# Performance work log

Measured on AMD Instinct MI355X. Metric: run time of the kernel, lower is better.

The kernel has to match this reference:

```python
import jax, jax.numpy as jnp
import numpy as np

SHIFT_HZ = 20.0
SAMPLE_RATE = 16000
N_FFT = 512
SHIFT_BINS = SHIFT_HZ / (SAMPLE_RATE / N_FFT)  # 0.64 bins
EPS = 1e-08


def setup_inputs() -> dict:
    key = jax.random.key(0)
    # log-magnitude spectrogram [B, 1, F, T]
    x = jax.random.normal(key, (32, 1, 257, 4096), dtype=jnp.float32)
    return {"x": x}


def reference(x):
    B, C, F, T = x.shape
    x_lin = jnp.power(10.0, x[:, 0])  # [B, F, T] linear magnitude

    f = jnp.arange(F, dtype=jnp.float32)
    target = f + SHIFT_BINS                     # source bin (fractional)
    f_low = jnp.floor(target)
    f_high = jnp.ceil(target)
    alpha = (target - f_low).astype(x.dtype)    # interp weight; 0 when integer

    valid = (target >= 0) & (target < F) & (f_low < F) & (f_high < F)
    lo = jnp.clip(f_low.astype(jnp.int32), 0, F - 1)
    hi = jnp.clip(f_high.astype(jnp.int32), 0, F - 1)

    # gather along frequency axis + linear interp (alpha==0 reduces to copy)
    interp = ((1.0 - alpha)[None, :, None] * jnp.take(x_lin, lo, axis=1)
              + alpha[None, :, None] * jnp.take(x_lin, hi, axis=1))
    shifted = jnp.where(valid[None, :, None], interp, 0.0)

    return jnp.log10(shifted + EPS)[:, None]    # [B, 1, F, T]
```

## Files before the change

kernel.cpp:

```cpp
#include <hip/hip_runtime.h>

#define B_DIM 32
#define F_DIM 257
#define T_DIM 4096
#define EPS_F 1e-8f

#define LOG2_10  3.32192809488736234787f
#define LOG10_2  0.30102999566398119521f

typedef float f32x4 __attribute__((ext_vector_type(4)));

__device__ __forceinline__ float pow10_fast(float v) {
    return __builtin_amdgcn_exp2f(v * LOG2_10);
}

__device__ __forceinline__ float log10_fast(float v) {
    return __builtin_amdgcn_logf(v) * LOG10_2;
}

__global__ __launch_bounds__(256) void freq_shift_kernel(
        const float* __restrict__ x, float* __restrict__ out) {
    const int bf = blockIdx.x;
    const int f  = bf % F_DIM;
    const long long base = (long long)bf * T_DIM;
    const int tid = threadIdx.x;

    f32x4* __restrict__ orow = (f32x4*)(out + base);

    if (f == F_DIM - 1) {
        const float cv = log10_fast(EPS_F);
        f32x4 v;
        v.x = cv; v.y = cv; v.z = cv; v.w = cv;
#pragma unroll
        for (int i = 0; i < T_DIM / 4 / 256; ++i)
            __builtin_nontemporal_store(v, orow + i * 256 + tid);
        return;
    }

    const f32x4* __restrict__ row0 = (const f32x4*)(x + base);
    const f32x4* __restrict__ row1 = (const f32x4*)(x + base + T_DIM);

    const float ff     = (float)f;
    const float target = ff + 0.64f;
    const float alpha  = target - ff;
    const float beta   = 1.0f - alpha;

    f32x4 va[4], vb[4];
#pragma unroll
    for (int i = 0; i < 4; ++i) va[i] = row0[i * 256 + tid];
#pragma unroll
    for (int i = 0; i < 4; ++i) vb[i] = row1[i * 256 + tid];

#pragma unroll
    for (int i = 0; i < 4; ++i) {
        f32x4 r;
        r.x = log10_fast(beta * pow10_fast(va[i].x) + alpha * pow10_fast(vb[i].x) + EPS_F);
        r.y = log10_fast(beta * pow10_fast(va[i].y) + alpha * pow10_fast(vb[i].y) + EPS_F);
        r.z = log10_fast(beta * pow10_fast(va[i].z) + alpha * pow10_fast(vb[i].z) + EPS_F);
        r.w = log10_fast(beta * pow10_fast(va[i].w) + alpha * pow10_fast(vb[i].w) + EPS_F);
        __builtin_nontemporal_store(r, orow + i * 256 + tid);
    }
}

extern "C" void kernel_launch(void* const* d_in, const int* in_sizes, int n_in,
                              void* d_out, int out_size, void* d_ws, size_t ws_size,
                              hipStream_t stream) {
    const float* x = (const float*)d_in[0];
    float* out = (float*)d_out;
    dim3 grid(B_DIM * F_DIM);
    dim3 block(256);
    freq_shift_kernel<<<grid, block, 0, stream>>>(x, out);
}
```

Before: 224.3 us.

## Tile 8 frequency rows per block to reuse pow10 and loads, remap blocks across XCDs

Each block now processes 8 consecutive frequency rows over half the time axis. It loads 9 input rows once and carries the pow10 of the previous row forward, so every input row is read and exponentiated once instead of twice. Block IDs are remapped so that contiguous work chunks land on the same XCD, which aims to improve L2 locality. The cost is more registers per thread and far fewer blocks (2048 instead of 8224), which may reduce latency hiding.

```diff
diff --git a/kernel.cpp b/kernel.cpp
--- a/kernel.cpp
+++ b/kernel.cpp
@@ -8,57 +8,78 @@
 #define LOG2_10  3.32192809488736234787f
 #define LOG10_2  0.30102999566398119521f
 
+#define ROWS 8
+#define FBLKS 32
+#define TCHUNKS 2
+#define TCHUNK_F (T_DIM / TCHUNKS)
+#define ROWV (T_DIM / 4)
+#define NBLK (B_DIM * FBLKS * TCHUNKS)
+#define XCD_CHUNK (NBLK / 8)
+
 typedef float f32x4 __attribute__((ext_vector_type(4)));
 
 __device__ __forceinline__ float pow10_fast(float v) {
     return __builtin_amdgcn_exp2f(v * LOG2_10);
 }
-
 __device__ __forceinline__ float log10_fast(float v) {
     return __builtin_amdgcn_logf(v) * LOG10_2;
+}
+__device__ __forceinline__ f32x4 pow10_4(f32x4 v) {
+    f32x4 r;
+    r.x = pow10_fast(v.x); r.y = pow10_fast(v.y);
+    r.z = pow10_fast(v.z); r.w = pow10_fast(v.w);
+    return r;
 }
 
 __global__ __launch_bounds__(256) void freq_shift_kernel(
         const float* __restrict__ x, float* __restrict__ out) {
-    const int bf = blockIdx.x;
-    const int f  = bf % F_DIM;
-    const long long base = (long long)bf * T_DIM;
+    const int bid = blockIdx.x;
+    const int id  = (bid & 7) * XCD_CHUNK + (bid >> 3);
+
+    const int b   = id >> 6;
+    const int rem = id & 63;
+    const int tc  = rem >> 5;
+    const int fb  = rem & 31;
+    const int f0  = fb * ROWS;
     const int tid = threadIdx.x;
 
-    f32x4* __restrict__ orow = (f32x4*)(out + base);
+    const long long base = ((long long)(b * F_DIM + f0)) * T_DIM + (long long)tc * TCHUNK_F;
+    const f32x4* __restrict__ xin = (const f32x4*)(x + base);
+    f32x4*       __restrict__ o   = (f32x4*)(out + base);
 
-    if (f == F_DIM - 1) {
-        const float cv = log10_fast(EPS_F);
-        f32x4 v;
-        v.x = cv; v.y = cv; v.z = cv; v.w = cv;
 #pragma unroll
-        for (int i = 0; i < T_DIM / 4 / 256; ++i)
-            __builtin_nontemporal_store(v, orow + i * 256 + tid);
-        return;
+    for (int half = 0; half < 2; ++half) {
+        const int c = tid + half * 256;
+
+        f32x4 v[ROWS + 1];
+#pragma unroll
+        for (int r = 0; r <= ROWS; ++r) v[r] = xin[r * ROWV + c];
+
+        f32x4 pprev = pow10_4(v[0]);
+#pragma unroll
+        for (int r = 0; r < ROWS; ++r) {
+            const float ff    = (float)(f0 + r);
+            const float alpha = (ff + 0.64f) - ff;
+            const float beta  = 1.0f - alpha;
+
+            const f32x4 pcur = pow10_4(v[r + 1]);
+            f32x4 res;
+            res.x = log10_fast(beta * pprev.x + alpha * pcur.x + EPS_F);
+            res.y = log10_fast(beta * pprev.y + alpha * pcur.y + EPS_F);
+            res.z = log10_fast(beta * pprev.z + alpha * pcur.z + EPS_F);
+            res.w = log10_fast(beta * pprev.w + alpha * pcur.w + EPS_F);
+            __builtin_nontemporal_store(res, o + r * ROWV + c);
+            pprev = pcur;
+        }
     }
 
-    const f32x4* __restrict__ row0 = (const f32x4*)(x + base);
-    const f32x4* __restrict__ row1 = (const f32x4*)(x + base + T_DIM);
-
-    const float ff     = (float)f;
-    const float target = ff + 0.64f;
-    const float alpha  = target - ff;
-    const float beta   = 1.0f - alpha;
-
-    f32x4 va[4], vb[4];
-#pragma unroll
-    for (int i = 0; i < 4; ++i) va[i] = row0[i * 256 + tid];
-#pragma unroll
-    for (int i = 0; i < 4; ++i) vb[i] = row1[i * 256 + tid];
-
-#pragma unroll
-    for (int i = 0; i < 4; ++i) {
-        f32x4 r;
-        r.x = log10_fast(beta * pow10_fast(va[i].x) + alpha * pow10_fast(vb[i].x) + EPS_F);
-        r.y = log10_fast(beta * pow10_fast(va[i].y) + alpha * pow10_fast(vb[i].y) + EPS_F);
-        r.z = log10_fast(beta * pow10_fast(va[i].z) + alpha * pow10_fast(vb[i].z) + EPS_F);
-        r.w = log10_fast(beta * pow10_fast(va[i].w) + alpha * pow10_fast(vb[i].w) + EPS_F);
-        __builtin_nontemporal_store(r, orow + i * 256 + tid);
+    if (fb == FBLKS - 1) {
+        const float cv = log10_fast(EPS_F);
+        f32x4 vv; vv.x = cv; vv.y = cv; vv.z = cv; vv.w = cv;
+        f32x4* orow = (f32x4*)(out + ((long long)(b * F_DIM + 256)) * T_DIM
+                               + (long long)tc * TCHUNK_F);
+        __builtin_nontemporal_store(vv, orow + tid);
+        __builtin_nontemporal_store(vv, orow + tid + 256);
     }
 }
 
@@ -67,7 +88,7 @@
                               hipStream_t stream) {
     const float* x = (const float*)d_in[0];
     float* out = (float*)d_out;
-    dim3 grid(B_DIM * F_DIM);
+    dim3 grid(NBLK);
     dim3 block(256);
     freq_shift_kernel<<<grid, block, 0, stream>>>(x, out);
 }
```

Measured after the change: 237.0 us. 5.7% more time.

## Process four rows per block with double-buffered loads and XCD-aware block mapping

Applied to the files above, without the earlier changes.

Each block now handles four consecutive frequency rows and issues the loads for the next row before computing the current one, hiding memory latency. Block IDs are remapped so each XCD gets a contiguous chunk of rows. Adjacent rows, which share an input row, then hit the same L2. The cost is fewer blocks in flight and more registers per thread for the double buffers, which may lower occupancy.

```diff
diff --git a/kernel.cpp b/kernel.cpp
--- a/kernel.cpp
+++ b/kernel.cpp
@@ -8,57 +8,76 @@
 #define LOG2_10  3.32192809488736234787f
 #define LOG10_2  0.30102999566398119521f
 
+#define TASKS 4
+#define NBLK  (B_DIM * F_DIM / TASKS)
+#define ROWV  (T_DIM / 4)
+#define XCD_CHUNK (NBLK / 8)
+
 typedef float f32x4 __attribute__((ext_vector_type(4)));
 
 __device__ __forceinline__ float pow10_fast(float v) {
     return __builtin_amdgcn_exp2f(v * LOG2_10);
 }
-
 __device__ __forceinline__ float log10_fast(float v) {
     return __builtin_amdgcn_logf(v) * LOG10_2;
 }
 
 __global__ __launch_bounds__(256) void freq_shift_kernel(
         const float* __restrict__ x, float* __restrict__ out) {
-    const int bf = blockIdx.x;
-    const int f  = bf % F_DIM;
-    const long long base = (long long)bf * T_DIM;
     const int tid = threadIdx.x;
+    const int bid = blockIdx.x;
+    const int id  = (bid & 7) * XCD_CHUNK + (bid >> 3);
+    const int t0  = id * TASKS;
 
-    f32x4* __restrict__ orow = (f32x4*)(out + base);
+    f32x4 va[2][4], vb[2][4];
 
-    if (f == F_DIM - 1) {
-        const float cv = log10_fast(EPS_F);
-        f32x4 v;
-        v.x = cv; v.y = cv; v.z = cv; v.w = cv;
+    auto issue = [&](int task) {
+        const int bf = t0 + task;
+        const int f  = bf % F_DIM;
+        const long long base = (long long)bf * T_DIM;
+        const f32x4* __restrict__ r0 = (const f32x4*)(x + base);
+        const f32x4* __restrict__ r1 = (f == F_DIM - 1) ? r0 : r0 + ROWV;
+        const int buf = task & 1;
 #pragma unroll
-        for (int i = 0; i < T_DIM / 4 / 256; ++i)
-            __builtin_nontemporal_store(v, orow + i * 256 + tid);
-        return;
-    }
+        for (int i = 0; i < 4; ++i) va[buf][i] = r0[i * 256 + tid];
+#pragma unroll
+        for (int i = 0; i < 4; ++i) vb[buf][i] = r1[i * 256 + tid];
+    };
 
-    const f32x4* __restrict__ row0 = (const f32x4*)(x + base);
-    const f32x4* __restrict__ row1 = (const f32x4*)(x + base + T_DIM);
+    issue(0);
+#pragma unroll
+    for (int t = 0; t < TASKS; ++t) {
+        if (t + 1 < TASKS) issue(t + 1);
 
-    const float ff     = (float)f;
-    const float target = ff + 0.64f;
-    const float alpha  = target - ff;
-    const float beta   = 1.0f - alpha;
+        const int bf = t0 + t;
+        const int f  = bf % F_DIM;
+        f32x4* __restrict__ orow = (f32x4*)(out + (long long)bf * T_DIM);
 
-    f32x4 va[4], vb[4];
+        if (f == F_DIM - 1) {
+            const float cv = log10_fast(EPS_F);
+            f32x4 v; v.x = cv; v.y = cv; v.z = cv; v.w = cv;
 #pragma unroll
-    for (int i = 0; i < 4; ++i) va[i] = row0[i * 256 + tid];
-#pragma unroll
-    for (int i = 0; i < 4; ++i) vb[i] = row1[i * 256 + tid];
+            for (int i = 0; i < 4; ++i)
+                __builtin_nontemporal_store(v, orow + i * 256 + tid);
+            continue;
+        }
+
+        const float ff    = (float)f;
+        const float alpha = (ff + 0.64f) - ff;
+        const float beta  = 1.0f - alpha;
+        const int   buf   = t & 1;
 
 #pragma unroll
-    for (int i = 0; i < 4; ++i) {
-        f32x4 r;
-        r.x = log10_fast(beta * pow10_fast(va[i].x) + alpha * pow10_fast(vb[i].x) + EPS_F);
-        r.y = log10_fast(beta * pow10_fast(va[i].y) + alpha * pow10_fast(vb[i].y) + EPS_F);
-        r.z = log10_fast(beta * pow10_fast(va[i].z) + alpha * pow10_fast(vb[i].z) + EPS_F);
-        r.w = log10_fast(beta * pow10_fast(va[i].w) + alpha * pow10_fast(vb[i].w) + EPS_F);
-        __builtin_nontemporal_store(r, orow + i * 256 + tid);
+        for (int i = 0; i < 4; ++i) {
+            const f32x4 a = va[buf][i];
+            const f32x4 b = vb[buf][i];
+            f32x4 r;
+            r.x = log10_fast(beta * pow10_fast(a.x) + alpha * pow10_fast(b.x) + EPS_F);
+            r.y = log10_fast(beta * pow10_fast(a.y) + alpha * pow10_fast(b.y) + EPS_F);
+            r.z = log10_fast(beta * pow10_fast(a.z) + alpha * pow10_fast(b.z) + EPS_F);
+            r.w = log10_fast(beta * pow10_fast(a.w) + alpha * pow10_fast(b.w) + EPS_F);
+            __builtin_nontemporal_store(r, orow + i * 256 + tid);
+        }
     }
 }
 
@@ -67,7 +86,7 @@
                               hipStream_t stream) {
     const float* x = (const float*)d_in[0];
     float* out = (float*)d_out;
-    dim3 grid(B_DIM * F_DIM);
+    dim3 grid(NBLK);
     dim3 block(256);
     freq_shift_kernel<<<grid, block, 0, stream>>>(x, out);
 }
```

New measurement: 244.1 us. +8.8%, slower.
